# Kernel tuning notes

Hardware: AMD Instinct MI355X
Metric: run time of the kernel (lower is better)

The kernel has to match this reference:

```python
import jax, jax.numpy as jnp
import numpy as np

PATCH = 16
B, C, H, W = 4, 3, 512, 512
N = 4096  # patches per image


def setup_inputs() -> dict:
    key = jax.random.key(0)
    k1, k2, k3, k4 = jax.random.split(key, 4)
    fuse = jax.random.normal(k1, (B, C, H, W), jnp.float32)
    img1 = jax.random.normal(k2, (B, C, H, W), jnp.float32)
    img2 = jax.random.normal(k3, (B, C, H, W), jnp.float32)
    # valid top-left (h, w) so h+PATCH <= H, w+PATCH <= W
    coords = jax.random.randint(k4, (B, N, 2), 0, H - PATCH + 1, dtype=jnp.int32)
    return {"fuse": fuse, "img1": img1, "img2": img2, "coords": coords}


def _extract_patches(image, coords):
    # image: [B,C,H,W], coords: [B,N,2] -> patches [B,C,N,P] with P=PATCH*PATCH
    c = image.shape[1]

    def one(img_b, hw):
        p = jax.lax.dynamic_slice(img_b, (0, hw[0], hw[1]), (c, PATCH, PATCH))
        return p.reshape(c, PATCH * PATCH)

    pat = jax.vmap(jax.vmap(one, in_axes=(None, 0)), in_axes=(0, 0))(image, coords)  # [B,N,C,P]
    return jnp.transpose(pat, (0, 2, 1, 3))  # [B,C,N,P]


def reference(fuse, img1, img2, coords):
    pf = _extract_patches(fuse, coords)
    p1 = _extract_patches(img1, coords)
    p2 = _extract_patches(img2, coords)
    mu1 = jnp.mean(p1, axis=-1, keepdims=True)
    mu2 = jnp.mean(p2, axis=-1, keepdims=True)
    sd1 = jnp.sqrt(jnp.mean((p1 - mu1) ** 2, axis=-1, keepdims=True))
    sd2 = jnp.sqrt(jnp.mean((p2 - mu2) ** 2, axis=-1, keepdims=True))
    denom = sd1 + sd2 + 1e-6
    target = (sd1 / denom) * p1 + (sd2 / denom) * p2
    return jnp.mean(jnp.abs(pf - target))
```

## Files before the change

### kernel.cpp

```cpp
#include <hip/hip_runtime.h>

#define BD 4
#define CD 3
#define HD 512
#define WD 512
#define NPAT 4096
#define NP (BD * NPAT)
#define PLANE (HD * WD)
#define NBLK (NP / 4)
#define TOTAL_ELEMS (4.0 * 3.0 * 4096.0 * 256.0)

typedef float f4 __attribute__((ext_vector_type(4), aligned(4)));

__global__ __launch_bounds__(256) void build_order(
    const int* __restrict__ coords, unsigned int* __restrict__ order)
{
    __shared__ unsigned short cnt[256][16];
    __shared__ unsigned short part[16][17];
    __shared__ unsigned int   base[16];

    const int t   = threadIdx.x;
    const int b   = blockIdx.x;
    const int key16 = t >> 4;
    const int sub   = t & 15;

    #pragma unroll
    for (int k = 0; k < 16; ++k) cnt[t][k] = 0;
    __syncthreads();

    const int2* c2 = (const int2*)coords;
    unsigned int pk[16];
    #pragma unroll
    for (int i = 0; i < 16; ++i) {
        const int p = (b << 12) + (i << 8) + t;
        const int2 hw = c2[p];
        pk[i] = ((unsigned)b << 18) | ((unsigned)hw.x << 9) | (unsigned)hw.y;
        cnt[t][hw.x >> 5]++;
    }
    __syncthreads();

    unsigned run = 0;
    #pragma unroll
    for (int tt = sub * 16; tt < sub * 16 + 16; ++tt) run += cnt[tt][key16];
    part[key16][sub] = (unsigned short)run;
    __syncthreads();

    if (t < 16) {
        unsigned r = 0;
        #pragma unroll
        for (int s = 0; s < 16; ++s) { unsigned v = part[t][s]; part[t][s] = (unsigned short)r; r += v; }
        base[t] = r;
    }
    __syncthreads();
    if (t == 0) {
        unsigned r = 0;
        #pragma unroll
        for (int k = 0; k < 16; ++k) { unsigned v = base[k]; base[k] = r; r += v; }
    }
    __syncthreads();

    {
        unsigned r = part[key16][sub];
        #pragma unroll
        for (int tt = sub * 16; tt < sub * 16 + 16; ++tt) {
            unsigned v = cnt[tt][key16]; cnt[tt][key16] = (unsigned short)r; r += v;
        }
    }
    __syncthreads();

    #pragma unroll
    for (int i = 0; i < 16; ++i) {
        const unsigned key = (pk[i] >> 14) & 15;
        const unsigned pos = base[key] + cnt[t][key];
        cnt[t][key]++;
        order[(b << 12) + pos] = pk[i];
    }
}

__global__ __launch_bounds__(256) void patch_stage1(
    const float* __restrict__ fuse,
    const float* __restrict__ img1,
    const float* __restrict__ img2,
    const unsigned int* __restrict__ order,
    float* __restrict__ partials)
{
    const int lane = threadIdx.x & 63;
    const int wave = threadIdx.x >> 6;
    const int bid     = blockIdx.x;
    const int slotblk = (bid & 7) * (NBLK / 8) + (bid >> 3);
    const int slot    = slotblk * 4 + wave;

    const unsigned v = order[slot];
    const int w = v & 511;
    const int h = (v >> 9) & 511;
    const int b = v >> 18;

    const size_t pbase = ((size_t)(b * CD) * HD + h) * WD + w
                       + (size_t)(lane >> 2) * WD + (size_t)((lane & 3) * 4);

    f4 vf[3], v1[3], v2[3];
    #pragma unroll
    for (int c = 0; c < CD; ++c) {
        const size_t idx = pbase + (size_t)c * PLANE;
        vf[c] = *(const f4*)(fuse + idx);
        v1[c] = *(const f4*)(img1 + idx);
        v2[c] = *(const f4*)(img2 + idx);
    }

    float s1[3], q1[3], s2[3], q2[3];
    #pragma unroll
    for (int c = 0; c < CD; ++c) {
        s1[c] = v1[c].x + v1[c].y + v1[c].z + v1[c].w;
        q1[c] = v1[c].x * v1[c].x + v1[c].y * v1[c].y
              + v1[c].z * v1[c].z + v1[c].w * v1[c].w;
        s2[c] = v2[c].x + v2[c].y + v2[c].z + v2[c].w;
        q2[c] = v2[c].x * v2[c].x + v2[c].y * v2[c].y
              + v2[c].z * v2[c].z + v2[c].w * v2[c].w;
    }

    #pragma unroll
    for (int off = 32; off >= 1; off >>= 1) {
        #pragma unroll
        for (int c = 0; c < CD; ++c) {
            s1[c] += __shfl_xor(s1[c], off, 64);
            q1[c] += __shfl_xor(q1[c], off, 64);
            s2[c] += __shfl_xor(s2[c], off, 64);
            q2[c] += __shfl_xor(q2[c], off, 64);
        }
    }

    float acc = 0.f;
    const float inv = 1.f / 256.f;
    #pragma unroll
    for (int c = 0; c < CD; ++c) {
        const float mu1 = s1[c] * inv;
        const float mu2 = s2[c] * inv;
        const float sd1 = sqrtf(fmaxf(q1[c] * inv - mu1 * mu1, 0.f));
        const float sd2 = sqrtf(fmaxf(q2[c] * inv - mu2 * mu2, 0.f));
        const float denom = sd1 + sd2 + 1e-6f;
        const float w1 = sd1 / denom;
        const float w2 = sd2 / denom;
        acc += fabsf(vf[c].x - (w1 * v1[c].x + w2 * v2[c].x))
             + fabsf(vf[c].y - (w1 * v1[c].y + w2 * v2[c].y))
             + fabsf(vf[c].z - (w1 * v1[c].z + w2 * v2[c].z))
             + fabsf(vf[c].w - (w1 * v1[c].w + w2 * v2[c].w));
    }

    #pragma unroll
    for (int off = 32; off >= 1; off >>= 1)
        acc += __shfl_xor(acc, off, 64);

    __shared__ float partsm[4];
    if (lane == 0) partsm[wave] = acc;
    __syncthreads();
    if (threadIdx.x == 0)
        partials[bid] = partsm[0] + partsm[1] + partsm[2] + partsm[3];
}

__global__ __launch_bounds__(256) void patch_stage2(
    const float* __restrict__ partials, float* __restrict__ out)
{
    float s = 0.f;
    for (int i = threadIdx.x; i < NBLK; i += 256)
        s += partials[i];

    #pragma unroll
    for (int off = 32; off >= 1; off >>= 1)
        s += __shfl_xor(s, off, 64);

    __shared__ float partsm[4];
    const int lane = threadIdx.x & 63;
    const int wave = threadIdx.x >> 6;
    if (lane == 0) partsm[wave] = s;
    __syncthreads();
    if (threadIdx.x == 0)
        out[0] = (partsm[0] + partsm[1] + partsm[2] + partsm[3]) * (float)(1.0 / TOTAL_ELEMS);
}

extern "C" void kernel_launch(void* const* d_in, const int* in_sizes, int n_in,
                              void* d_out, int out_size, void* d_ws, size_t ws_size,
                              hipStream_t stream) {
    const float* fuse   = (const float*)d_in[0];
    const float* img1   = (const float*)d_in[1];
    const float* img2   = (const float*)d_in[2];
    const int*   coords = (const int*)d_in[3];
    float* out = (float*)d_out;

    unsigned int* order    = (unsigned int*)d_ws;
    float*        partials = (float*)((char*)d_ws + NP * 4);

    build_order<<<BD, 256, 0, stream>>>(coords, order);
    patch_stage1<<<NBLK, 256, 0, stream>>>(fuse, img1, img2, order, partials);
    patch_stage2<<<1, 256, 0, stream>>>(partials, out);
}
```

Baseline: 34.12 us.

## Prefetch image planes with warm-up blocks and fuse final reduction via atomics

Adds 128 extra leading blocks to the patch kernel that stream every image plane once to pull it into the cache hierarchy before or alongside the random patch reads. Replaces the separate final reduction kernel with a per-block atomicAdd into the zeroed output, dropping one launch but adding a memset. Also pads the shared count array in the sort kernel to reduce bank conflicts. The warm-up reads extra bandwidth and the atomic makes the summation order nondeterministic.

```diff
diff --git a/kernel.cpp b/kernel.cpp
--- a/kernel.cpp
+++ b/kernel.cpp
@@ -7,7 +7,8 @@
 #define NPAT 4096
 #define NP (BD * NPAT)
 #define PLANE (HD * WD)
-#define NBLK (NP / 4)
+#define NPB (NP / 4)
+#define NWARM 128
 #define TOTAL_ELEMS (4.0 * 3.0 * 4096.0 * 256.0)
 
 typedef float f4 __attribute__((ext_vector_type(4), aligned(4)));
@@ -15,7 +16,7 @@
 __global__ __launch_bounds__(256) void build_order(
     const int* __restrict__ coords, unsigned int* __restrict__ order)
 {
-    __shared__ unsigned short cnt[256][16];
+    __shared__ unsigned short cnt[256][18];
     __shared__ unsigned short part[16][17];
     __shared__ unsigned int   base[16];
 
@@ -82,12 +83,37 @@
     const float* __restrict__ img1,
     const float* __restrict__ img2,
     const unsigned int* __restrict__ order,
-    float* __restrict__ partials)
+    float* __restrict__ out)
 {
+    const int bid = blockIdx.x;
+
+    if (bid < NWARM) {
+        const int xcd = bid & 7;
+        const int sub = bid >> 3;
+        const int b   = xcd >> 1;
+        const int r0  = (xcd & 1) * 256;
+        const float* imgs[3] = { fuse, img1, img2 };
+        float s = 0.f;
+        #pragma unroll
+        for (int im = 0; im < 3; ++im) {
+            #pragma unroll
+            for (int c = 0; c < CD; ++c) {
+                const f4* p = (const f4*)(imgs[im] + ((size_t)((b * CD + c) * HD + r0)) * WD);
+                #pragma unroll
+                for (int k = 0; k < 8; ++k) {
+                    const f4 v = p[k * 4096 + sub * 256 + threadIdx.x];
+                    s += v.x + v.y + v.z + v.w;
+                }
+            }
+        }
+        asm volatile("" :: "v"(s));
+        return;
+    }
+
     const int lane = threadIdx.x & 63;
     const int wave = threadIdx.x >> 6;
-    const int bid     = blockIdx.x;
-    const int slotblk = (bid & 7) * (NBLK / 8) + (bid >> 3);
+    const int pbid = bid - NWARM;
+    const int slotblk = (pbid & 7) * (NPB / 8) + (pbid >> 3);
     const int slot    = slotblk * 4 + wave;
 
     const unsigned v = order[slot];
@@ -154,27 +180,8 @@
     if (lane == 0) partsm[wave] = acc;
     __syncthreads();
     if (threadIdx.x == 0)
-        partials[bid] = partsm[0] + partsm[1] + partsm[2] + partsm[3];
-}
-
-__global__ __launch_bounds__(256) void patch_stage2(
-    const float* __restrict__ partials, float* __restrict__ out)
-{
-    float s = 0.f;
-    for (int i = threadIdx.x; i < NBLK; i += 256)
-        s += partials[i];
-
-    #pragma unroll
-    for (int off = 32; off >= 1; off >>= 1)
-        s += __shfl_xor(s, off, 64);
-
-    __shared__ float partsm[4];
-    const int lane = threadIdx.x & 63;
-    const int wave = threadIdx.x >> 6;
-    if (lane == 0) partsm[wave] = s;
-    __syncthreads();
-    if (threadIdx.x == 0)
-        out[0] = (partsm[0] + partsm[1] + partsm[2] + partsm[3]) * (float)(1.0 / TOTAL_ELEMS);
+        atomicAdd(out, (partsm[0] + partsm[1] + partsm[2] + partsm[3])
+                        * (float)(1.0 / TOTAL_ELEMS));
 }
 
 extern "C" void kernel_launch(void* const* d_in, const int* in_sizes, int n_in,
@@ -186,10 +193,9 @@
     const int*   coords = (const int*)d_in[3];
     float* out = (float*)d_out;
 
-    unsigned int* order    = (unsigned int*)d_ws;
-    float*        partials = (float*)((char*)d_ws + NP * 4);
-
+    unsigned int* order = (unsigned int*)d_ws;
+
+    hipMemsetAsync(out, 0, sizeof(float), stream);
     build_order<<<BD, 256, 0, stream>>>(coords, order);
-    patch_stage1<<<NBLK, 256, 0, stream>>>(fuse, img1, img2, order, partials);
-    patch_stage2<<<1, 256, 0, stream>>>(partials, out);
+    patch_stage1<<<NWARM + NPB, 256, 0, stream>>>(fuse, img1, img2, order, out);
 }
```

Measured after the change: 72.71 us. 2.13x slower.

## Map one patch row per lane, fold final reduction via last-block atomic

Applied to the files above, without the earlier changes.

Each lane now loads a full 16-float row of a patch, so a wave covers four patches and a block covers sixteen. This cuts the block count and shortens the shuffle reductions to 16-lane groups. The separate stage-2 kernel is replaced by a last-block-done pattern: an atomic counter, zeroed by a memset each launch, tells the final block to sum the partials. The shared count array in the sort kernel is padded to reduce bank conflicts. In exchange there is an extra memset launch and fence and atomic overhead, and each lane's row-wise loads are less coalesced across the wave.

```diff
diff --git a/kernel.cpp b/kernel.cpp
--- a/kernel.cpp
+++ b/kernel.cpp
@@ -7,7 +7,9 @@
 #define NPAT 4096
 #define NP (BD * NPAT)
 #define PLANE (HD * WD)
-#define NBLK (NP / 4)
+#define PPW 4
+#define PPB 16
+#define NBLK (NP / PPB)
 #define TOTAL_ELEMS (4.0 * 3.0 * 4096.0 * 256.0)
 
 typedef float f4 __attribute__((ext_vector_type(4), aligned(4)));
@@ -15,12 +17,12 @@
 __global__ __launch_bounds__(256) void build_order(
     const int* __restrict__ coords, unsigned int* __restrict__ order)
 {
-    __shared__ unsigned short cnt[256][16];
+    __shared__ unsigned short cnt[256][18];
     __shared__ unsigned short part[16][17];
     __shared__ unsigned int   base[16];
 
-    const int t   = threadIdx.x;
-    const int b   = blockIdx.x;
+    const int t = threadIdx.x;
+    const int b = blockIdx.x;
     const int key16 = t >> 4;
     const int sub   = t & 15;
 
@@ -82,68 +84,73 @@
     const float* __restrict__ img1,
     const float* __restrict__ img2,
     const unsigned int* __restrict__ order,
-    float* __restrict__ partials)
+    float* __restrict__ partials,
+    unsigned int* __restrict__ donecnt,
+    float* __restrict__ out)
 {
     const int lane = threadIdx.x & 63;
     const int wave = threadIdx.x >> 6;
-    const int bid     = blockIdx.x;
+    const int bid  = blockIdx.x;
     const int slotblk = (bid & 7) * (NBLK / 8) + (bid >> 3);
-    const int slot    = slotblk * 4 + wave;
+    const int slot    = slotblk * PPB + wave * PPW + (lane >> 4);
 
     const unsigned v = order[slot];
     const int w = v & 511;
     const int h = (v >> 9) & 511;
     const int b = v >> 18;
-
-    const size_t pbase = ((size_t)(b * CD) * HD + h) * WD + w
-                       + (size_t)(lane >> 2) * WD + (size_t)((lane & 3) * 4);
-
-    f4 vf[3], v1[3], v2[3];
-    #pragma unroll
-    for (int c = 0; c < CD; ++c) {
-        const size_t idx = pbase + (size_t)c * PLANE;
-        vf[c] = *(const f4*)(fuse + idx);
-        v1[c] = *(const f4*)(img1 + idx);
-        v2[c] = *(const f4*)(img2 + idx);
-    }
-
-    float s1[3], q1[3], s2[3], q2[3];
-    #pragma unroll
-    for (int c = 0; c < CD; ++c) {
-        s1[c] = v1[c].x + v1[c].y + v1[c].z + v1[c].w;
-        q1[c] = v1[c].x * v1[c].x + v1[c].y * v1[c].y
-              + v1[c].z * v1[c].z + v1[c].w * v1[c].w;
-        s2[c] = v2[c].x + v2[c].y + v2[c].z + v2[c].w;
-        q2[c] = v2[c].x * v2[c].x + v2[c].y * v2[c].y
-              + v2[c].z * v2[c].z + v2[c].w * v2[c].w;
-    }
-
-    #pragma unroll
-    for (int off = 32; off >= 1; off >>= 1) {
-        #pragma unroll
-        for (int c = 0; c < CD; ++c) {
-            s1[c] += __shfl_xor(s1[c], off, 64);
-            q1[c] += __shfl_xor(q1[c], off, 64);
-            s2[c] += __shfl_xor(s2[c], off, 64);
-            q2[c] += __shfl_xor(q2[c], off, 64);
-        }
-    }
+    const int r = lane & 15;
+
+    const size_t pb = (size_t)(b * CD) * PLANE + (size_t)(h + r) * WD + w;
 
     float acc = 0.f;
     const float inv = 1.f / 256.f;
+
     #pragma unroll
     for (int c = 0; c < CD; ++c) {
-        const float mu1 = s1[c] * inv;
-        const float mu2 = s2[c] * inv;
-        const float sd1 = sqrtf(fmaxf(q1[c] * inv - mu1 * mu1, 0.f));
-        const float sd2 = sqrtf(fmaxf(q2[c] * inv - mu2 * mu2, 0.f));
-        const float denom = sd1 + sd2 + 1e-6f;
-        const float w1 = sd1 / denom;
-        const float w2 = sd2 / denom;
-        acc += fabsf(vf[c].x - (w1 * v1[c].x + w2 * v2[c].x))
-             + fabsf(vf[c].y - (w1 * v1[c].y + w2 * v2[c].y))
-             + fabsf(vf[c].z - (w1 * v1[c].z + w2 * v2[c].z))
-             + fabsf(vf[c].w - (w1 * v1[c].w + w2 * v2[c].w));
+        const float* pf = fuse + pb + (size_t)c * PLANE;
+        const float* p1 = img1 + pb + (size_t)c * PLANE;
+        const float* p2 = img2 + pb + (size_t)c * PLANE;
+
+        const f4 vf0 = *(const f4*)(pf);      const f4 vf1 = *(const f4*)(pf + 4);
+        const f4 vf2 = *(const f4*)(pf + 8);  const f4 vf3 = *(const f4*)(pf + 12);
+        const f4 a0  = *(const f4*)(p1);      const f4 a1  = *(const f4*)(p1 + 4);
+        const f4 a2  = *(const f4*)(p1 + 8);  const f4 a3  = *(const f4*)(p1 + 12);
+        const f4 b0  = *(const f4*)(p2);      const f4 b1  = *(const f4*)(p2 + 4);
+        const f4 b2  = *(const f4*)(p2 + 8);  const f4 b3  = *(const f4*)(p2 + 12);
+
+        const f4 sa = (a0 + a1) + (a2 + a3);
+        float s1 = sa.x + sa.y + sa.z + sa.w;
+        f4 qa = a0 * a0; qa += a1 * a1; qa += a2 * a2; qa += a3 * a3;
+        float q1 = qa.x + qa.y + qa.z + qa.w;
+        const f4 sb = (b0 + b1) + (b2 + b3);
+        float s2 = sb.x + sb.y + sb.z + sb.w;
+        f4 qb = b0 * b0; qb += b1 * b1; qb += b2 * b2; qb += b3 * b3;
+        float q2 = qb.x + qb.y + qb.z + qb.w;
+
+        #pragma unroll
+        for (int off = 8; off >= 1; off >>= 1) {
+            s1 += __shfl_xor(s1, off, 64);
+            q1 += __shfl_xor(q1, off, 64);
+            s2 += __shfl_xor(s2, off, 64);
+            q2 += __shfl_xor(q2, off, 64);
+        }
+
+        const float mu1 = s1 * inv;
+        const float mu2 = s2 * inv;
+        const float sd1 = sqrtf(fmaxf(q1 * inv - mu1 * mu1, 0.f));
+        const float sd2 = sqrtf(fmaxf(q2 * inv - mu2 * mu2, 0.f));
+        const float den = sd1 + sd2 + 1e-6f;
+        const float w1 = sd1 / den;
+        const float w2 = sd2 / den;
+
+        const f4 d0 = vf0 - (w1 * a0 + w2 * b0);
+        const f4 d1 = vf1 - (w1 * a1 + w2 * b1);
+        const f4 d2 = vf2 - (w1 * a2 + w2 * b2);
+        const f4 d3 = vf3 - (w1 * a3 + w2 * b3);
+        acc += (fabsf(d0.x) + fabsf(d0.y)) + (fabsf(d0.z) + fabsf(d0.w))
+             + (fabsf(d1.x) + fabsf(d1.y)) + (fabsf(d1.z) + fabsf(d1.w))
+             + (fabsf(d2.x) + fabsf(d2.y)) + (fabsf(d2.z) + fabsf(d2.w))
+             + (fabsf(d3.x) + fabsf(d3.y)) + (fabsf(d3.z) + fabsf(d3.w));
     }
 
     #pragma unroll
@@ -151,30 +158,31 @@
         acc += __shfl_xor(acc, off, 64);
 
     __shared__ float partsm[4];
+    __shared__ unsigned isLast;
     if (lane == 0) partsm[wave] = acc;
     __syncthreads();
-    if (threadIdx.x == 0)
+    if (threadIdx.x == 0) {
         partials[bid] = partsm[0] + partsm[1] + partsm[2] + partsm[3];
-}
-
-__global__ __launch_bounds__(256) void patch_stage2(
-    const float* __restrict__ partials, float* __restrict__ out)
-{
-    float s = 0.f;
-    for (int i = threadIdx.x; i < NBLK; i += 256)
-        s += partials[i];
-
-    #pragma unroll
-    for (int off = 32; off >= 1; off >>= 1)
-        s += __shfl_xor(s, off, 64);
-
-    __shared__ float partsm[4];
-    const int lane = threadIdx.x & 63;
-    const int wave = threadIdx.x >> 6;
-    if (lane == 0) partsm[wave] = s;
-    __syncthreads();
-    if (threadIdx.x == 0)
-        out[0] = (partsm[0] + partsm[1] + partsm[2] + partsm[3]) * (float)(1.0 / TOTAL_ELEMS);
+        __threadfence();
+        isLast = (atomicAdd(donecnt, 1u) == NBLK - 1) ? 1u : 0u;
+    }
+    __syncthreads();
+
+    if (isLast) {
+        __threadfence();
+        float s = 0.f;
+        for (int i = threadIdx.x; i < NBLK; i += 256)
+            s += partials[i];
+        #pragma unroll
+        for (int off = 32; off >= 1; off >>= 1)
+            s += __shfl_xor(s, off, 64);
+        __syncthreads();
+        if (lane == 0) partsm[wave] = s;
+        __syncthreads();
+        if (threadIdx.x == 0)
+            out[0] = (partsm[0] + partsm[1] + partsm[2] + partsm[3])
+                     * (float)(1.0 / TOTAL_ELEMS);
+    }
 }
 
 extern "C" void kernel_launch(void* const* d_in, const int* in_sizes, int n_in,
@@ -188,8 +196,10 @@
 
     unsigned int* order    = (unsigned int*)d_ws;
     float*        partials = (float*)((char*)d_ws + NP * 4);
-
+    unsigned int* donecnt  = (unsigned int*)((char*)d_ws + NP * 4 + NBLK * 4);
+
+    hipMemsetAsync(donecnt, 0, sizeof(unsigned int), stream);
     build_order<<<BD, 256, 0, stream>>>(coords, order);
-    patch_stage1<<<NBLK, 256, 0, stream>>>(fuse, img1, img2, order, partials);
-    patch_stage2<<<1, 256, 0, stream>>>(partials, out);
+    patch_stage1<<<NBLK, 256, 0, stream>>>(fuse, img1, img2, order,
+                                           partials, donecnt, out);
 }
```

Measured after the change: 71.43 us. 2.09x slower.
